# Optimization experiments

Hardware: AMD Instinct MI355X
Metric: run time of the kernel (lower is better)

## Reference

```python
import jax, jax.numpy as jnp
import numpy as np

B, S, H, V, T, NS, NB, NSW = 16, 200, 400, 25000, 8, 30, 3, 36


def setup_inputs() -> dict:
    key = jax.random.key(0)
    ks = jax.random.split(key, 12)
    return {
        "encoded_hidden": jax.random.normal(ks[0], (1, B, H), jnp.float32),
        "encoded_outputs": jax.random.normal(ks[1], (B, S, H), jnp.float32),
        "story": jax.random.randint(ks[2], (B, S), 0, V),
        "target_batches": jax.random.randint(ks[3], (B, NS, T), 0, V),
        "slot_dom_idx": jax.random.randint(ks[4], (NS,), 0, NSW),
        "slot_slot_idx": jax.random.randint(ks[5], (NS,), 0, NSW),
        "emb_W": jax.random.normal(ks[6], (V, H), jnp.float32) * 0.05,
        "slot_emb_W": jax.random.normal(ks[7], (NSW, H), jnp.float32) * 0.1,
        "gru_W_ih": jax.random.normal(ks[8], (3 * H, H), jnp.float32) * 0.05,
        "gru_W_hh": jax.random.normal(ks[9], (3 * H, H), jnp.float32) * 0.05,
        "gru_b_ih": jnp.zeros((3 * H,), jnp.float32),
        "gru_b_hh": jnp.zeros((3 * H,), jnp.float32),
        "W_ratio_w": jax.random.normal(ks[10], (1, 3 * H), jnp.float32) * 0.05,
        "W_ratio_b": jnp.zeros((1,), jnp.float32),
        "W_gate_w": jax.random.normal(ks[11], (NB, H), jnp.float32) * 0.05,
        "W_gate_b": jnp.zeros((NB,), jnp.float32),
    }


def reference(encoded_hidden, encoded_outputs, story, target_batches,
              slot_dom_idx, slot_slot_idx, emb_W, slot_emb_W,
              gru_W_ih, gru_W_hh, gru_b_ih, gru_b_hh,
              W_ratio_w, W_ratio_b, W_gate_w, W_gate_b):
    b, s, h = encoded_outputs.shape
    ns = slot_dom_idx.shape[0]
    v = emb_W.shape[0]
    t = target_batches.shape[2]
    bs = ns * b  # flattened slot*batch dim (parallel decode over slots)

    # slot embedding = domain_emb + slot_emb, broadcast over batch
    slot_emb = slot_emb_W[slot_dom_idx] + slot_emb_W[slot_slot_idx]        # [ns,h]
    dec_in0 = jnp.broadcast_to(slot_emb[:, None, :], (ns, b, h)).reshape(bs, h)
    h0 = jnp.tile(encoded_hidden[0], (ns, 1))                              # [bs,h]
    enc = jnp.tile(encoded_outputs, (ns, 1, 1))                            # [bs,s,h]
    pad_mask = jnp.tile(story == 0, (ns, 1))                               # [bs,s]
    story_rep = jnp.tile(story, (ns, 1))                                   # [bs,s]
    # teacher forcing targets, slot-major flatten: [bs, t]
    tf = jnp.transpose(target_batches, (1, 0, 2)).reshape(bs, t)
    rows = jnp.arange(bs)

    def gru_cell(x, hid):
        gx = x @ gru_W_ih.T + gru_b_ih
        gh = hid @ gru_W_hh.T + gru_b_hh
        r = jax.nn.sigmoid(gx[:, :h] + gh[:, :h])
        z = jax.nn.sigmoid(gx[:, h:2 * h] + gh[:, h:2 * h])
        n = jnp.tanh(gx[:, 2 * h:] + r * gh[:, 2 * h:])
        return (1.0 - z) * n + z * hid

    def step(carry, tgt_t):
        hid, x = carry
        hid = gru_cell(x, hid)                                             # [bs,h]
        scores = jnp.einsum('bh,bsh->bs', hid, enc)
        scores = jnp.where(pad_mask, -jnp.inf, scores)
        prob = jax.nn.softmax(scores, axis=1)                              # [bs,s]
        ctx = jnp.einsum('bs,bsh->bh', prob, enc)                          # [bs,h]
        p_vocab = jax.nn.softmax(hid @ emb_W.T, axis=1)                    # [bs,v]
        switch = jax.nn.sigmoid(
            jnp.concatenate([hid, ctx, x], axis=-1) @ W_ratio_w.T + W_ratio_b)  # [bs,1]
        p_ctx = jnp.zeros((bs, v), p_vocab.dtype).at[rows[:, None], story_rep].add(prob)
        final = (1.0 - switch) * p_ctx + switch * p_vocab                  # [bs,v]
        x_next = emb_W[tgt_t]                                              # teacher forcing
        return (hid, x_next), (final, ctx)

    (_, _), (finals, ctxs) = jax.lax.scan(step, (h0, dec_in0), tf.T)
    all_point = jnp.transpose(finals.reshape(t, ns, b, v), (1, 2, 0, 3))   # [ns,b,t,v]
    all_gate = (ctxs[0] @ W_gate_w.T + W_gate_b).reshape(ns, b, -1)        # [ns,b,nb_gate]
    return all_point, all_gate
```

## Files before the change

### kernel.cpp

```cpp
#include <hip/hip_runtime.h>
#include <math.h>

#define B_   16
#define S_   200
#define H_   400
#define V_   25000
#define T_   8
#define NS_  30
#define NB_  3
#define BS_  480

#define KP_  448
#define MP_  512
#define NP_  25088
#define NG_  1280
#define MA_  3840
#define NVT_ (NP_/128)
#define PSL_ 200

typedef unsigned short u16;
typedef __attribute__((ext_vector_type(4))) float f32x4;
typedef __attribute__((ext_vector_type(8))) short short8;

__device__ __forceinline__ u16 f2bf(float f) {
    unsigned u = __float_as_uint(f);
    u += 0x7FFFu + ((u >> 16) & 1u);
    return (u16)(u >> 16);
}
__device__ __forceinline__ float bf2f(u16 v) {
    return __uint_as_float(((unsigned)v) << 16);
}
__device__ __forceinline__ float sigm(float x) {
    return 1.f / (1.f + __expf(-x));
}
__device__ __forceinline__ float ftanh(float x) {
    float e2 = __expf(2.f * x);
    return 1.f - 2.f / (e2 + 1.f);
}
__device__ __forceinline__ float wred_sum(float v) {
    v += __shfl_xor(v, 32); v += __shfl_xor(v, 16); v += __shfl_xor(v, 8);
    v += __shfl_xor(v, 4);  v += __shfl_xor(v, 2);  v += __shfl_xor(v, 1);
    return v;
}
__device__ __forceinline__ float wred_max(float v) {
    v = fmaxf(v, __shfl_xor(v, 32)); v = fmaxf(v, __shfl_xor(v, 16));
    v = fmaxf(v, __shfl_xor(v, 8));  v = fmaxf(v, __shfl_xor(v, 4));
    v = fmaxf(v, __shfl_xor(v, 2));  v = fmaxf(v, __shfl_xor(v, 1));
    return v;
}
__device__ __forceinline__ void gload_lds16(const void* g, void* l) {
    __builtin_amdgcn_global_load_lds(
        (const __attribute__((address_space(1))) void*)g,
        (__attribute__((address_space(3))) void*)l, 16, 0, 0);
}

#define MFMA_SETUP()                                                          \
    const int wid = tid >> 6, lane = tid & 63;                                \
    const int wr = wid >> 1, wc = wid & 1;                                    \
    f32x4 acc[4][4] = {};                                                     \
    const int lcol = ((lane & 7) ^ ((lane >> 3) & 7)) * 8;                    \
    const int lr = lane & 15, lg = lane >> 4, lx = lane & 7;                  \
    const int sA0 = (lg ^ lx) * 8, sA1 = ((4 + lg) ^ lx) * 8;

__global__ void prep_all(const float* __restrict__ eh, const float* __restrict__ embW,
                         const float* __restrict__ Wih, const float* __restrict__ Whh,
                         const float* __restrict__ sembW, const int* __restrict__ tb,
                         const int* __restrict__ dom, const int* __restrict__ sli,
                         float* __restrict__ hid, u16* __restrict__ Ab,
                         u16* __restrict__ Bb, u16* __restrict__ Wihb, u16* __restrict__ Whhb,
                         float* __restrict__ x_all, u16* __restrict__ Xb_all) {
    const int R0 = MP_ * KP_;
    const int CB = NP_ * (KP_ / 8), CG = NG_ * (KP_ / 8);
    const int R1 = R0 + CB + 2 * CG;
    const int R2 = R1 + MA_ * (KP_ / 8);
    int i = blockIdx.x * 256 + threadIdx.x;
    if (i < R0) {
        int row = i / KP_, d = i - row * KP_;
        u16 v = 0;
        if (row < BS_ && d < H_) {
            float h = eh[(row % B_) * H_ + d];
            hid[row * H_ + d] = h;
            v = f2bf(h);
        }
        Ab[i] = v;
    } else if (i < R1) {
        int j = i - R0;
        const float* src; u16* dst; int rows;
        if (j < CB) { src = embW; dst = Bb; rows = V_; }
        else if (j < CB + CG) { src = Wih; dst = Wihb; rows = 3 * H_; j -= CB; }
        else { src = Whh; dst = Whhb; rows = 3 * H_; j -= CB + CG; }
        int row = j / (KP_ / 8), c8 = (j - row * (KP_ / 8)) * 8;
        short8 o = {};
        if (row < rows && c8 < H_) {
            const float4* s = reinterpret_cast<const float4*>(src + (size_t)row * H_ + c8);
            float4 a = s[0], b = s[1];
            o[0] = (short)f2bf(a.x); o[1] = (short)f2bf(a.y);
            o[2] = (short)f2bf(a.z); o[3] = (short)f2bf(a.w);
            o[4] = (short)f2bf(b.x); o[5] = (short)f2bf(b.y);
            o[6] = (short)f2bf(b.z); o[7] = (short)f2bf(b.w);
        }
        *reinterpret_cast<short8*>(dst + (size_t)row * KP_ + c8) = o;
    } else if (i < R2) {
        int j = i - R1;
        int row = j / (KP_ / 8), c8 = (j - row * (KP_ / 8)) * 8;
        int t = row / BS_, r = row - t * BS_;
        int batch = r % B_, slot = r / B_;
        short8 o = {};
        if (c8 < H_) {
            float4 a, b;
            if (t == 0) {
                const float4* s0 = reinterpret_cast<const float4*>(sembW + dom[slot] * H_ + c8);
                const float4* s1 = reinterpret_cast<const float4*>(sembW + sli[slot] * H_ + c8);
                float4 x0 = s0[0], x1 = s0[1], y0 = s1[0], y1 = s1[1];
                a = make_float4(x0.x + y0.x, x0.y + y0.y, x0.z + y0.z, x0.w + y0.w);
                b = make_float4(x1.x + y1.x, x1.y + y1.y, x1.z + y1.z, x1.w + y1.w);
            } else {
                int tok = tb[(batch * NS_ + slot) * T_ + (t - 1)];
                const float4* s = reinterpret_cast<const float4*>(embW + (size_t)tok * H_ + c8);
                a = s[0]; b = s[1];
            }
            o[0] = (short)f2bf(a.x); o[1] = (short)f2bf(a.y);
            o[2] = (short)f2bf(a.z); o[3] = (short)f2bf(a.w);
            o[4] = (short)f2bf(b.x); o[5] = (short)f2bf(b.y);
            o[6] = (short)f2bf(b.z); o[7] = (short)f2bf(b.w);
            *reinterpret_cast<float4*>(x_all + (size_t)row * H_ + c8) = a;
            *reinterpret_cast<float4*>(x_all + (size_t)row * H_ + c8 + 4) = b;
        }
        *reinterpret_cast<short8*>(Xb_all + (size_t)row * KP_ + c8) = o;
    }
}

__global__ __launch_bounds__(256)
void gemm_setup(const u16* __restrict__ Xb_all, const u16* __restrict__ Abuf,
                const u16* __restrict__ Wihb, const u16* __restrict__ Whhb,
                float* __restrict__ gx_all, float* __restrict__ gh) {
    __shared__ u16 As[128 * 64];
    __shared__ u16 Bs[128 * 64];
    const int tid = threadIdx.x;
    const bool mainp = blockIdx.y < (MA_ / 128);
    const int m0 = (mainp ? blockIdx.y : blockIdx.y - MA_ / 128) * 128;
    const int n0 = blockIdx.x * 128;
    const u16* A = mainp ? Xb_all : Abuf;
    const u16* Bw = mainp ? Wihb : Whhb;
    float* C = mainp ? gx_all : gh;
    const int Mlim = mainp ? MA_ : BS_;

    MFMA_SETUP();
    const u16* Ag = A + (size_t)(m0 + wid * 32 + (lane >> 3)) * KP_ + lcol;
    const u16* Bg = Bw + (size_t)(n0 + wid * 32 + (lane >> 3)) * KP_ + lcol;

    for (int kt = 0; kt < 7; ++kt) {
        const int k0 = kt * 64;
        #pragma unroll
        for (int is = 0; is < 4; ++is) {
            gload_lds16(Ag + (size_t)is * 8 * KP_ + k0, &As[(wid * 32 + is * 8) * 64]);
            gload_lds16(Bg + (size_t)is * 8 * KP_ + k0, &Bs[(wid * 32 + is * 8) * 64]);
        }
        __syncthreads();
        short8 af[4][2], bfr[4][2];
        #pragma unroll
        for (int i = 0; i < 4; ++i) {
            int ra = (wr * 64 + i * 16 + lr) * 64;
            af[i][0] = *reinterpret_cast<const short8*>(&As[ra + sA0]);
            af[i][1] = *reinterpret_cast<const short8*>(&As[ra + sA1]);
            int rb = (wc * 64 + i * 16 + lr) * 64;
            bfr[i][0] = *reinterpret_cast<const short8*>(&Bs[rb + sA0]);
            bfr[i][1] = *reinterpret_cast<const short8*>(&Bs[rb + sA1]);
        }
        #pragma unroll
        for (int h = 0; h < 2; ++h)
            #pragma unroll
            for (int i = 0; i < 4; ++i)
                #pragma unroll
                for (int j = 0; j < 4; ++j)
                    acc[i][j] = __builtin_amdgcn_mfma_f32_16x16x32_bf16(
                        af[i][h], bfr[j][h], acc[i][j], 0, 0, 0);
        __syncthreads();
    }
    const int m_base = m0 + wr * 64 + lg * 4;
    const int n_base = n0 + wc * 64 + lr;
    #pragma unroll
    for (int i = 0; i < 4; ++i)
        #pragma unroll
        for (int r = 0; r < 4; ++r) {
            int m = m_base + i * 16 + r;
            if (m >= Mlim) continue;
            #pragma unroll
            for (int j = 0; j < 4; ++j) {
                int n = n_base + j * 16;
                if (n < 3 * H_) C[(size_t)m * 3 * H_ + n] = acc[i][j][r];
            }
        }
}

__global__ __launch_bounds__(256, 2)
void vocab_gh(const u16* __restrict__ A, const u16* __restrict__ Bb,
              const u16* __restrict__ Whhb, u16* __restrict__ pb,
              float* __restrict__ psum, float* __restrict__ gh) {
    __shared__ u16 As[256 * 64];
    __shared__ u16 Bs[2][128 * 64];
    __shared__ float sred[2][256];
    const int bid = blockIdx.x;
    const int tid = threadIdx.x;
    const int xcd = bid & 7, idx = bid >> 3;
    const int lin = (xcd < 4) ? (xcd * 52 + idx) : (208 + (xcd - 4) * 51 + idx);
    const int ntall = lin >> 1, mt = lin & 1;
    const bool isv = (ntall < NVT_);
    const int n0 = (isv ? ntall : ntall - NVT_) * 128;
    const int m0 = mt * 256;
    const u16* Bsrc = isv ? Bb : Whhb;

    const int wid = tid >> 6, lane = tid & 63;
    const int wr = wid >> 1, wc = wid & 1;
    f32x4 acc[8][4] = {};
    const int lcol = ((lane & 7) ^ ((lane >> 3) & 7)) * 8;
    const int lr = lane & 15, lg = lane >> 4, lx = lane & 7;
    const int sA0 = (lg ^ lx) * 8, sA1 = ((4 + lg) ^ lx) * 8;
    const u16* Ag = A + (size_t)(m0 + wid * 64 + (lane >> 3)) * KP_ + lcol;
    const u16* Bg = Bsrc + (size_t)(n0 + wid * 32 + (lane >> 3)) * KP_ + lcol;

    #pragma unroll
    for (int is = 0; is < 4; ++is)
        gload_lds16(Bg + (size_t)is * 8 * KP_, &Bs[0][(wid * 32 + is * 8) * 64]);

    for (int kt = 0; kt < 7; ++kt) {
        const int k0 = kt * 64, cur = kt & 1;
        #pragma unroll
        for (int is = 0; is < 8; ++is)
            gload_lds16(Ag + (size_t)is * 8 * KP_ + k0, &As[(wid * 64 + is * 8) * 64]);
        if (kt < 6) {
            #pragma unroll
            for (int is = 0; is < 4; ++is)
                gload_lds16(Bg + (size_t)is * 8 * KP_ + k0 + 64,
                            &Bs[cur ^ 1][(wid * 32 + is * 8) * 64]);
            asm volatile("s_waitcnt vmcnt(4)" ::: "memory");
        } else {
            asm volatile("s_waitcnt vmcnt(0)" ::: "memory");
        }
        __builtin_amdgcn_sched_barrier(0);
        __builtin_amdgcn_s_barrier();
        const u16* Bsl = Bs[cur];
        #pragma unroll
        for (int h = 0; h < 2; ++h) {
            const int sA = h ? sA1 : sA0;
            short8 af[8], bf[4];
            #pragma unroll
            for (int i = 0; i < 8; ++i)
                af[i] = *reinterpret_cast<const short8*>(&As[(wr * 128 + i * 16 + lr) * 64 + sA]);
            #pragma unroll
            for (int j = 0; j < 4; ++j)
                bf[j] = *reinterpret_cast<const short8*>(&Bsl[(wc * 64 + j * 16 + lr) * 64 + sA]);
            #pragma unroll
            for (int i = 0; i < 8; ++i)
                #pragma unroll
                for (int j = 0; j < 4; ++j)
                    acc[i][j] = __builtin_amdgcn_mfma_f32_16x16x32_bf16(
                        af[i], bf[j], acc[i][j], 0, 0, 0);
        }
        __builtin_amdgcn_s_barrier();
    }

    const int m_base = m0 + wr * 128 + lg * 4;
    const int n_base = n0 + wc * 64 + lr;
    if (isv) {
        #pragma unroll
        for (int i = 0; i < 8; ++i) {
            #pragma unroll
            for (int r = 0; r < 4; ++r) {
                int m = m_base + i * 16 + r;
                float js = 0.f;
                #pragma unroll
                for (int j = 0; j < 4; ++j) {
                    int n = n_base + j * 16;
                    float e = __expf(acc[i][j][r]);
                    if (m < BS_ && n < V_) {
                        pb[(size_t)m * V_ + n] = f2bf(e);
                        js += e;
                    }
                }
                js += __shfl_xor(js, 1);
                js += __shfl_xor(js, 2);
                js += __shfl_xor(js, 4);
                js += __shfl_xor(js, 8);
                if ((lane & 15) == 0) sred[wc][m - m0] = js;
            }
        }
        __syncthreads();
        {
            int m = m0 + tid;
            psum[(size_t)m * PSL_ + ntall] = sred[0][tid] + sred[1][tid];
        }
    } else {
        #pragma unroll
        for (int i = 0; i < 8; ++i)
            #pragma unroll
            for (int r = 0; r < 4; ++r) {
                int m = m_base + i * 16 + r;
                if (m >= BS_) continue;
                #pragma unroll
                for (int j = 0; j < 4; ++j) {
                    int n = n_base + j * 16;
                    if (n < 3 * H_) gh[(size_t)m * 3 * H_ + n] = acc[i][j][r];
                }
            }
    }
}

__global__ __launch_bounds__(256)
void attn_fin(const float* __restrict__ gx_all, const float* __restrict__ gh,
              const float* __restrict__ bih, const float* __restrict__ bhh,
              float* __restrict__ hid, u16* __restrict__ Ab,
              const float* __restrict__ x_all,
              const float* __restrict__ enc, const int* __restrict__ story,
              const float* __restrict__ Wr, const float* __restrict__ Wrb,
              const float* __restrict__ Wg, const float* __restrict__ Wgb,
              float* __restrict__ prob_cur, float* __restrict__ sw_cur,
              float* __restrict__ gate_out,
              float* __restrict__ out, const u16* __restrict__ pb,
              const float* __restrict__ psum, const float* __restrict__ sw_prev,
              const float* __restrict__ prob_prev, int t) {
    const int bid = blockIdx.x;
    const int lin = (bid & 7) * 120 + (bid >> 3);
    const int work = lin >> 1, kind = lin & 1;
    const int tid = threadIdx.x, w = tid >> 6, l = tid & 63;
    __shared__ __align__(16) float hs[H_];
    __shared__ __align__(16) float xs[H_];
    __shared__ __align__(16) float cs[H_];
    __shared__ __align__(16) float cpart[4][H_];
    __shared__ float sc[S_];
    __shared__ float red[16];

    if (kind == 1) {
        if (t == 0) return;
        const int row = work, batch = row % B_;
        float rs = (tid < NVT_) ? psum[(size_t)row * PSL_ + tid] : 0.f;
        rs = wred_sum(rs);
        if (l == 0) red[w] = rs;
        __syncthreads();
        float denom = red[0] + red[1] + red[2] + red[3];
        float swv = sw_prev[row];
        float scl = swv / denom;
        const u16* ps = pb + (size_t)row * V_;
        float* p = out + ((size_t)row * T_ + (t - 1)) * V_;
        for (int v = tid * 8; v < V_; v += 256 * 8) {
            short8 in = *reinterpret_cast<const short8*>(ps + v);
            float4 o0, o1;
            o0.x = bf2f((u16)in[0]) * scl; o0.y = bf2f((u16)in[1]) * scl;
            o0.z = bf2f((u16)in[2]) * scl; o0.w = bf2f((u16)in[3]) * scl;
            o1.x = bf2f((u16)in[4]) * scl; o1.y = bf2f((u16)in[5]) * scl;
            o1.z = bf2f((u16)in[6]) * scl; o1.w = bf2f((u16)in[7]) * scl;
            *reinterpret_cast<float4*>(p + v) = o0;
            *reinterpret_cast<float4*>(p + v + 4) = o1;
        }
        __syncthreads();
        float om = 1.f - swv;
        for (int s = tid; s < S_; s += 256) {
            int tok = story[batch * S_ + s];
            atomicAdd(p + tok, om * prob_prev[(size_t)row * S_ + s]);
        }
        return;
    }

    const int batch = work / 30, slot = work - batch * 30;
    const int row = slot * B_ + batch;

    const float* gxr = gx_all + ((size_t)t * BS_ + row) * 3 * H_;
    const float* ghr = gh + (size_t)row * 3 * H_;
    const float* xr  = x_all + ((size_t)t * BS_ + row) * H_;
    for (int d = tid; d < H_; d += 256) {
        float r = sigm(gxr[d] + bih[d] + ghr[d] + bhh[d]);
        float z = sigm(gxr[H_ + d] + bih[H_ + d] + ghr[H_ + d] + bhh[H_ + d]);
        float n = ftanh(gxr[2 * H_ + d] + bih[2 * H_ + d] + r * (ghr[2 * H_ + d] + bhh[2 * H_ + d]));
        float h = (1.f - z) * n + z * hid[(size_t)row * H_ + d];
        hs[d] = h;
        hid[(size_t)row * H_ + d] = h;
        Ab[(size_t)row * KP_ + d] = f2bf(h);
        xs[d] = xr[d];
    }
    __syncthreads();

    const float* encb = enc + (size_t)batch * S_ * H_;
    {
        float4 hv1 = *reinterpret_cast<const float4*>(&hs[l * 4]);
        float4 hv2 = make_float4(0.f, 0.f, 0.f, 0.f);
        if (l < 36) hv2 = *reinterpret_cast<const float4*>(&hs[256 + l * 4]);
        for (int k = 0; k < 50; k += 2) {
            int s0 = w * 50 + k;
            const float4* e0 = reinterpret_cast<const float4*>(encb + (size_t)s0 * H_);
            const float4* e1 = reinterpret_cast<const float4*>(encb + (size_t)(s0 + 1) * H_);
            float4 ev0 = e0[l], ev1 = e1[l];
            float p0 = ev0.x * hv1.x + ev0.y * hv1.y + ev0.z * hv1.z + ev0.w * hv1.w;
            float p1 = ev1.x * hv1.x + ev1.y * hv1.y + ev1.z * hv1.z + ev1.w * hv1.w;
            if (l < 36) {
                float4 f0 = e0[64 + l], f1 = e1[64 + l];
                p0 += f0.x * hv2.x + f0.y * hv2.y + f0.z * hv2.z + f0.w * hv2.w;
                p1 += f1.x * hv2.x + f1.y * hv2.y + f1.z * hv2.z + f1.w * hv2.w;
            }
            p0 = wred_sum(p0);
            p1 = wred_sum(p1);
            if (l == 0) {
                sc[s0]     = (story[batch * S_ + s0] == 0)     ? -1e30f : p0;
                sc[s0 + 1] = (story[batch * S_ + s0 + 1] == 0) ? -1e30f : p1;
            }
        }
    }
    __syncthreads();

    float v = (tid < S_) ? sc[tid] : -1e30f;
    float wm = wred_max(v);
    if (l == 0) red[w] = wm;
    __syncthreads();
    float mx = fmaxf(fmaxf(red[0], red[1]), fmaxf(red[2], red[3]));
    float e = (tid < S_) ? __expf(v - mx) : 0.f;
    float wsum = wred_sum(e);
    if (l == 0) red[4 + w] = wsum;
    __syncthreads();
    float inv = 1.f / (red[4] + red[5] + red[6] + red[7]);
    if (tid < S_) {
        float pv = e * inv;
        sc[tid] = pv;
        prob_cur[(size_t)row * S_ + tid] = pv;
    }
    __syncthreads();

    {
        const int s0 = w * 50;
        for (int d = l; d < H_; d += 64) {
            float a0 = 0.f, a1 = 0.f;
            for (int k = 0; k < 50; k += 2) {
                a0 += sc[s0 + k]     * encb[(size_t)(s0 + k) * H_ + d];
                a1 += sc[s0 + k + 1] * encb[(size_t)(s0 + k + 1) * H_ + d];
            }
            cpart[w][d] = a0 + a1;
        }
    }
    __syncthreads();
    for (int d = tid; d < H_; d += 256)
        cs[d] = cpart[0][d] + cpart[1][d] + cpart[2][d] + cpart[3][d];
    __syncthreads();

    float part = 0.f;
    for (int i = tid; i < 3 * H_; i += 256) {
        float xv = (i < H_) ? hs[i] : (i < 2 * H_) ? cs[i - H_] : xs[i - 2 * H_];
        part += xv * Wr[i];
    }
    part = wred_sum(part);
    if (l == 0) red[8 + w] = part;
    __syncthreads();
    if (tid == 0)
        sw_cur[row] = sigm(red[8] + red[9] + red[10] + red[11] + Wrb[0]);

    if (t == 0 && tid < NB_) {
        float acc = 0.f;
        for (int d = 0; d < H_; ++d) acc += cs[d] * Wg[tid * H_ + d];
        gate_out[(size_t)row * NB_ + tid] = acc + Wgb[tid];
    }
}

__global__ __launch_bounds__(256)
void scale_scatter(float* __restrict__ out, const u16* __restrict__ pb,
                   const float* __restrict__ psum, const float* __restrict__ sw,
                   const float* __restrict__ prob, const int* __restrict__ story) {
    const int row = blockIdx.x;
    const int tid = threadIdx.x, w = tid >> 6, l = tid & 63;
    __shared__ float red[4];
    float rs = (tid < NVT_) ? psum[(size_t)row * PSL_ + tid] : 0.f;
    rs = wred_sum(rs);
    if (l == 0) red[w] = rs;
    __syncthreads();
    float denom = red[0] + red[1] + red[2] + red[3];
    float swv = sw[row];
    float scl = swv / denom;
    const u16* ps = pb + (size_t)row * V_;
    float* p = out + ((size_t)row * T_ + (T_ - 1)) * V_;
    for (int v = tid * 8; v < V_; v += 256 * 8) {
        short8 in = *reinterpret_cast<const short8*>(ps + v);
        float4 o0, o1;
        o0.x = bf2f((u16)in[0]) * scl; o0.y = bf2f((u16)in[1]) * scl;
        o0.z = bf2f((u16)in[2]) * scl; o0.w = bf2f((u16)in[3]) * scl;
        o1.x = bf2f((u16)in[4]) * scl; o1.y = bf2f((u16)in[5]) * scl;
        o1.z = bf2f((u16)in[6]) * scl; o1.w = bf2f((u16)in[7]) * scl;
        *reinterpret_cast<float4*>(p + v) = o0;
        *reinterpret_cast<float4*>(p + v + 4) = o1;
    }
    __syncthreads();
    const int batch = row % B_;
    float om = 1.f - swv;
    for (int s = tid; s < S_; s += 256) {
        int tok = story[batch * S_ + s];
        atomicAdd(p + tok, om * prob[(size_t)row * S_ + s]);
    }
}

extern "C" void kernel_launch(void* const* d_in, const int* in_sizes, int n_in,
                              void* d_out, int out_size, void* d_ws, size_t ws_size,
                              hipStream_t stream) {
    const float* eh    = (const float*)d_in[0];
    const float* enc   = (const float*)d_in[1];
    const int*   story = (const int*)d_in[2];
    const int*   tb    = (const int*)d_in[3];
    const int*   dom   = (const int*)d_in[4];
    const int*   sli   = (const int*)d_in[5];
    const float* embW  = (const float*)d_in[6];
    const float* sembW = (const float*)d_in[7];
    const float* Wih   = (const float*)d_in[8];
    const float* Whh   = (const float*)d_in[9];
    const float* bih   = (const float*)d_in[10];
    const float* bhh   = (const float*)d_in[11];
    const float* Wr    = (const float*)d_in[12];
    const float* Wrb   = (const float*)d_in[13];
    const float* Wg    = (const float*)d_in[14];
    const float* Wgb   = (const float*)d_in[15];

    float* out = (float*)d_out;
    float* ws  = (float*)d_ws;

    float* gx_all = ws;
    float* gh     = gx_all + (size_t)MA_ * 3 * H_;
    float* hid    = gh + (size_t)BS_ * 3 * H_;
    float* x_all  = hid + (size_t)BS_ * H_;
    float* prob2  = x_all + (size_t)MA_ * H_;
    float* sw2    = prob2 + 2 * BS_ * S_;
    float* psum   = sw2 + 2 * BS_;
    u16* Ab     = (u16*)(psum + (size_t)MP_ * PSL_);
    u16* Xb_all = Ab + (size_t)MP_ * KP_;
    u16* Wihb   = Xb_all + (size_t)MA_ * KP_;
    u16* Whhb   = Wihb + (size_t)NG_ * KP_;
    u16* Bb     = Whhb + (size_t)NG_ * KP_;
    u16* pb     = Bb + (size_t)NP_ * KP_;
    size_t need = (size_t)((char*)(pb + (size_t)BS_ * V_) - (char*)ws);
    if (ws_size < need) return;

    float* gate_out = out + (size_t)NS_ * B_ * T_ * V_;

    {
        const int R2 = MP_ * KP_ + (NP_ + 2 * NG_) * (KP_ / 8) + MA_ * (KP_ / 8);
        prep_all<<<(R2 + 255) / 256, 256, 0, stream>>>(eh, embW, Wih, Whh, sembW, tb, dom, sli,
                                                       hid, Ab, Bb, Wihb, Whhb, x_all, Xb_all);
    }
    gemm_setup<<<dim3(NG_ / 128, MA_ / 128 + MP_ / 128), 256, 0, stream>>>(
        Xb_all, Ab, Wihb, Whhb, gx_all, gh);

    for (int t = 0; t < T_; ++t) {
        const int cur = t & 1, prev = cur ^ 1;
        attn_fin<<<960, 256, 0, stream>>>(gx_all, gh, bih, bhh, hid, Ab, x_all,
                                          enc, story, Wr, Wrb, Wg, Wgb,
                                          prob2 + cur * BS_ * S_, sw2 + cur * BS_,
                                          gate_out, out, pb, psum,
                                          sw2 + prev * BS_, prob2 + prev * BS_ * S_, t);
        vocab_gh<<<412, 256, 0, stream>>>(Ab, Bb, Whhb, pb, psum, gh);
    }
    {
        const int last = (T_ - 1) & 1;
        scale_scatter<<<BS_, 256, 0, stream>>>(out, pb, psum, sw2 + last * BS_,
                                               prob2 + last * BS_ * S_, story);
    }
}
```

Baseline: 770.1 us.

## Defer most of the input-gate GEMM into the first vocab_gh launch

The setup GEMM now computes only the first 4 row-tiles (512 rows) of the x·W_ih projection plus the h·W_hh tiles. The remaining 26 row-tiles (260 blocks) are appended as extra blocks to the first vocab_gh launch, so they run alongside the vocab GEMM instead of serialising before the decode loop. The shared 128x128 MFMA tile code is pulled into a helper function. Correctness relies on timestep 0 reading only the first 512 rows of gx_all. Extra blocks in vocab_gh could disturb its XCD block mapping or occupancy for that one launch.

```diff
diff --git a/kernel.cpp b/kernel.cpp
--- a/kernel.cpp
+++ b/kernel.cpp
@@ -54,13 +54,61 @@
         (__attribute__((address_space(3))) void*)l, 16, 0, 0);
 }
 
-#define MFMA_SETUP()                                                          \
-    const int wid = tid >> 6, lane = tid & 63;                                \
-    const int wr = wid >> 1, wc = wid & 1;                                    \
-    f32x4 acc[4][4] = {};                                                     \
-    const int lcol = ((lane & 7) ^ ((lane >> 3) & 7)) * 8;                    \
-    const int lr = lane & 15, lg = lane >> 4, lx = lane & 7;                  \
+__device__ __forceinline__ void tile128(const u16* __restrict__ A, const u16* __restrict__ Bw,
+                                        float* __restrict__ C, int m0, int n0, int Mlim, int Nlim,
+                                        u16* As, u16* Bs, int tid) {
+    const int wid = tid >> 6, lane = tid & 63;
+    const int wr = wid >> 1, wc = wid & 1;
+    f32x4 acc[4][4] = {};
+    const int lcol = ((lane & 7) ^ ((lane >> 3) & 7)) * 8;
+    const int lr = lane & 15, lg = lane >> 4, lx = lane & 7;
     const int sA0 = (lg ^ lx) * 8, sA1 = ((4 + lg) ^ lx) * 8;
+    const u16* Ag = A + (size_t)(m0 + wid * 32 + (lane >> 3)) * KP_ + lcol;
+    const u16* Bg = Bw + (size_t)(n0 + wid * 32 + (lane >> 3)) * KP_ + lcol;
+
+    for (int kt = 0; kt < 7; ++kt) {
+        const int k0 = kt * 64;
+        #pragma unroll
+        for (int is = 0; is < 4; ++is) {
+            gload_lds16(Ag + (size_t)is * 8 * KP_ + k0, &As[(wid * 32 + is * 8) * 64]);
+            gload_lds16(Bg + (size_t)is * 8 * KP_ + k0, &Bs[(wid * 32 + is * 8) * 64]);
+        }
+        __syncthreads();
+        short8 af[4][2], bfr[4][2];
+        #pragma unroll
+        for (int i = 0; i < 4; ++i) {
+            int ra = (wr * 64 + i * 16 + lr) * 64;
+            af[i][0] = *reinterpret_cast<const short8*>(&As[ra + sA0]);
+            af[i][1] = *reinterpret_cast<const short8*>(&As[ra + sA1]);
+            int rb = (wc * 64 + i * 16 + lr) * 64;
+            bfr[i][0] = *reinterpret_cast<const short8*>(&Bs[rb + sA0]);
+            bfr[i][1] = *reinterpret_cast<const short8*>(&Bs[rb + sA1]);
+        }
+        #pragma unroll
+        for (int h = 0; h < 2; ++h)
+            #pragma unroll
+            for (int i = 0; i < 4; ++i)
+                #pragma unroll
+                for (int j = 0; j < 4; ++j)
+                    acc[i][j] = __builtin_amdgcn_mfma_f32_16x16x32_bf16(
+                        af[i][h], bfr[j][h], acc[i][j], 0, 0, 0);
+        __syncthreads();
+    }
+    const int m_base = m0 + wr * 64 + lg * 4;
+    const int n_base = n0 + wc * 64 + lr;
+    #pragma unroll
+    for (int i = 0; i < 4; ++i)
+        #pragma unroll
+        for (int r = 0; r < 4; ++r) {
+            int m = m_base + i * 16 + r;
+            if (m >= Mlim) continue;
+            #pragma unroll
+            for (int j = 0; j < 4; ++j) {
+                int n = n_base + j * 16;
+                if (n < Nlim) C[(size_t)m * Nlim + n] = acc[i][j][r];
+            }
+        }
+}
 
 __global__ void prep_all(const float* __restrict__ eh, const float* __restrict__ embW,
                          const float* __restrict__ Wih, const float* __restrict__ Whh,
@@ -137,71 +185,35 @@
     __shared__ u16 As[128 * 64];
     __shared__ u16 Bs[128 * 64];
     const int tid = threadIdx.x;
-    const bool mainp = blockIdx.y < (MA_ / 128);
-    const int m0 = (mainp ? blockIdx.y : blockIdx.y - MA_ / 128) * 128;
+    const bool mainp = blockIdx.y < 4;
+    const int m0 = (mainp ? blockIdx.y : blockIdx.y - 4) * 128;
     const int n0 = blockIdx.x * 128;
-    const u16* A = mainp ? Xb_all : Abuf;
-    const u16* Bw = mainp ? Wihb : Whhb;
-    float* C = mainp ? gx_all : gh;
-    const int Mlim = mainp ? MA_ : BS_;
-
-    MFMA_SETUP();
-    const u16* Ag = A + (size_t)(m0 + wid * 32 + (lane >> 3)) * KP_ + lcol;
-    const u16* Bg = Bw + (size_t)(n0 + wid * 32 + (lane >> 3)) * KP_ + lcol;
-
-    for (int kt = 0; kt < 7; ++kt) {
-        const int k0 = kt * 64;
-        #pragma unroll
-        for (int is = 0; is < 4; ++is) {
-            gload_lds16(Ag + (size_t)is * 8 * KP_ + k0, &As[(wid * 32 + is * 8) * 64]);
-            gload_lds16(Bg + (size_t)is * 8 * KP_ + k0, &Bs[(wid * 32 + is * 8) * 64]);
-        }
-        __syncthreads();
-        short8 af[4][2], bfr[4][2];
-        #pragma unroll
-        for (int i = 0; i < 4; ++i) {
-            int ra = (wr * 64 + i * 16 + lr) * 64;
-            af[i][0] = *reinterpret_cast<const short8*>(&As[ra + sA0]);
-            af[i][1] = *reinterpret_cast<const short8*>(&As[ra + sA1]);
-            int rb = (wc * 64 + i * 16 + lr) * 64;
-            bfr[i][0] = *reinterpret_cast<const short8*>(&Bs[rb + sA0]);
-            bfr[i][1] = *reinterpret_cast<const short8*>(&Bs[rb + sA1]);
-        }
-        #pragma unroll
-        for (int h = 0; h < 2; ++h)
-            #pragma unroll
-            for (int i = 0; i < 4; ++i)
-                #pragma unroll
-                for (int j = 0; j < 4; ++j)
-                    acc[i][j] = __builtin_amdgcn_mfma_f32_16x16x32_bf16(
-                        af[i][h], bfr[j][h], acc[i][j], 0, 0, 0);
-        __syncthreads();
-    }
-    const int m_base = m0 + wr * 64 + lg * 4;
-    const int n_base = n0 + wc * 64 + lr;
-    #pragma unroll
-    for (int i = 0; i < 4; ++i)
-        #pragma unroll
-        for (int r = 0; r < 4; ++r) {
-            int m = m_base + i * 16 + r;
-            if (m >= Mlim) continue;
-            #pragma unroll
-            for (int j = 0; j < 4; ++j) {
-                int n = n_base + j * 16;
-                if (n < 3 * H_) C[(size_t)m * 3 * H_ + n] = acc[i][j][r];
-            }
-        }
+    if (mainp)
+        tile128(Xb_all, Wihb, gx_all, m0, n0, MA_, 3 * H_, As, Bs, tid);
+    else
+        tile128(Abuf, Whhb, gh, m0, n0, BS_, 3 * H_, As, Bs, tid);
 }
 
 __global__ __launch_bounds__(256, 2)
 void vocab_gh(const u16* __restrict__ A, const u16* __restrict__ Bb,
               const u16* __restrict__ Whhb, u16* __restrict__ pb,
-              float* __restrict__ psum, float* __restrict__ gh) {
+              float* __restrict__ psum, float* __restrict__ gh,
+              const u16* __restrict__ Xb_all, const u16* __restrict__ Wihb,
+              float* __restrict__ gx_all) {
     __shared__ u16 As[256 * 64];
     __shared__ u16 Bs[2][128 * 64];
     __shared__ float sred[2][256];
     const int bid = blockIdx.x;
     const int tid = threadIdx.x;
+
+    if (bid >= 412) {
+        const int e = bid - 412;
+        const int mt = 4 + e / 10, nt = e % 10;
+        tile128(Xb_all, Wihb, gx_all, mt * 128, nt * 128, MA_, 3 * H_,
+                As, (u16*)&Bs[0][0], tid);
+        return;
+    }
+
     const int xcd = bid & 7, idx = bid >> 3;
     const int lin = (xcd < 4) ? (xcd * 52 + idx) : (208 + (xcd - 4) * 51 + idx);
     const int ntall = lin >> 1, mt = lin & 1;
@@ -538,8 +550,7 @@
         prep_all<<<(R2 + 255) / 256, 256, 0, stream>>>(eh, embW, Wih, Whh, sembW, tb, dom, sli,
                                                        hid, Ab, Bb, Wihb, Whhb, x_all, Xb_all);
     }
-    gemm_setup<<<dim3(NG_ / 128, MA_ / 128 + MP_ / 128), 256, 0, stream>>>(
-        Xb_all, Ab, Wihb, Whhb, gx_all, gh);
+    gemm_setup<<<dim3(NG_ / 128, 8), 256, 0, stream>>>(Xb_all, Ab, Wihb, Whhb, gx_all, gh);
 
     for (int t = 0; t < T_; ++t) {
         const int cur = t & 1, prev = cur ^ 1;
@@ -548,7 +559,8 @@
                                           prob2 + cur * BS_ * S_, sw2 + cur * BS_,
                                           gate_out, out, pb, psum,
                                           sw2 + prev * BS_, prob2 + prev * BS_ * S_, t);
-        vocab_gh<<<412, 256, 0, stream>>>(Ab, Bb, Whhb, pb, psum, gh);
+        vocab_gh<<<(t == 0 ? 672 : 412), 256, 0, stream>>>(Ab, Bb, Whhb, pb, psum, gh,
+                                                           Xb_all, Wihb, gx_all);
     }
     {
         const int last = (T_ - 1) & 1;
```

New measurement: 776.7 us. About the same (+0.9%).
